# Performance work log

Hardware: AMD Instinct MI355X
Metric: run time of the kernel (lower is better)

The kernel has to match this reference:

```python
import jax, jax.numpy as jnp
import numpy as np

N = 50000       # nodes
E = 600000      # edges (before self-loops)
D_IN, D_H, D_OUT, D_E = 128, 128, 64, 8
NEG_SLOPE = 0.2


def _glorot(key, shape):
    fan = shape[0]
    return jax.random.normal(key, shape, dtype=jnp.float32) / jnp.sqrt(jnp.float32(fan))


def setup_inputs() -> dict:
    key = jax.random.key(0)
    ks = iter(jax.random.split(key, 32))
    inp = {
        "x": jax.random.normal(next(ks), (N, D_IN), dtype=jnp.float32),
        "edge_index": jax.random.randint(next(ks), (2, E), 0, N, dtype=jnp.int64),
        "edge_attr": jax.random.normal(next(ks), (E, D_E), dtype=jnp.float32),
    }
    dims = [(D_IN, D_H), (D_H, D_H), (D_H, D_OUT)]  # 3 GATConv layers, heads=1
    for i, (din, dout) in enumerate(dims):
        inp[f"W{i}"] = _glorot(next(ks), (din, dout))
        inp[f"as{i}"] = _glorot(next(ks), (dout,))
        inp[f"ad{i}"] = _glorot(next(ks), (dout,))
        inp[f"We{i}"] = _glorot(next(ks), (D_E, dout))
        inp[f"ae{i}"] = _glorot(next(ks), (dout,))
        inp[f"b{i}"] = jnp.zeros((dout,), dtype=jnp.float32)
    return inp


def _add_self_loops(src, dst, edge_attr, n):
    # PyG add_self_loops(fill_value='mean'): self-loop attr = mean of incoming edge attrs
    deg = jax.ops.segment_sum(jnp.ones_like(dst, dtype=edge_attr.dtype), dst, num_segments=n)
    mean_attr = jax.ops.segment_sum(edge_attr, dst, num_segments=n) / jnp.maximum(deg, 1.0)[:, None]
    loop = jnp.arange(n, dtype=src.dtype)
    return (jnp.concatenate([src, loop]),
            jnp.concatenate([dst, loop]),
            jnp.concatenate([edge_attr, mean_attr], axis=0))


def _gat_layer(x, src, dst, edge_attr, W, a_s, a_d, We, a_e, b, n):
    h = x @ W                                   # [N, C] linear projection
    alpha = (h @ a_s)[src] + (h @ a_d)[dst] + (edge_attr @ We) @ a_e   # [Etot]
    alpha = jax.nn.leaky_relu(alpha, NEG_SLOPE)
    m = jax.ops.segment_max(alpha, dst, num_segments=n)                # segment softmax over dst
    ex = jnp.exp(alpha - m[dst])
    denom = jax.ops.segment_sum(ex, dst, num_segments=n)
    w = ex / (denom[dst] + 1e-16)
    return jax.ops.segment_sum(h[src] * w[:, None], dst, num_segments=n) + b


def reference(x, edge_index, edge_attr,
              W0, as0, ad0, We0, ae0, b0,
              W1, as1, ad1, We1, ae1, b1,
              W2, as2, ad2, We2, ae2, b2):
    n = x.shape[0]
    src, dst, ea = _add_self_loops(edge_index[0], edge_index[1], edge_attr, n)
    h = jax.nn.relu(_gat_layer(x, src, dst, ea, W0, as0, ad0, We0, ae0, b0, n))
    h = jax.nn.relu(_gat_layer(h, src, dst, ea, W1, as1, ad1, We1, ae1, b1, n))
    return _gat_layer(h, src, dst, ea, W2, as2, ad2, We2, ae2, b2, n)
```

## Files before the change

kernel.cpp:

```cpp
#include <hip/hip_runtime.h>
#include <hip/hip_fp16.h>
#include <cstdint>

#define NEG_SLOPE 0.2f
#define LOG2E 1.4426950408889634f
#define MAXD 64


__global__ void k_zero(int* __restrict__ p, int n) {
    int i = blockIdx.x * blockDim.x + threadIdx.x;
    if (i < n) p[i] = 0;
}

__global__ void k_count_fill(const int* __restrict__ src, const int* __restrict__ dst,
                             const float* __restrict__ ea,
                             const float* __restrict__ We0, const float* __restrict__ ae0,
                             const float* __restrict__ We1, const float* __restrict__ ae1,
                             const float* __restrict__ We2, const float* __restrict__ ae2,
                             int* __restrict__ deg, ushort4* __restrict__ ed, int E) {
    __shared__ float swea[24];
    int tid = threadIdx.x;
    if (tid < 24) {
        int layer = tid >> 3, k = tid & 7;
        const float* We = layer == 0 ? We0 : (layer == 1 ? We1 : We2);
        const float* ae = layer == 0 ? ae0 : (layer == 1 ? ae1 : ae2);
        int D = layer == 2 ? 64 : 128;
        float s = 0.f;
        for (int t = 0; t < D; t++) s = fmaf(We[(size_t)k * D + t], ae[t], s);
        swea[tid] = s;
    }
    __syncthreads();
    int e = blockIdx.x * blockDim.x + tid;
    if (e >= E) return;
    int s = src[e];
    int d = dst[e];
    int r = atomicAdd(deg + d, 1);
    if (r > MAXD - 1) r = MAXD - 1;
    float4 a0 = *(const float4*)&ea[(size_t)e * 8];
    float4 a1 = *(const float4*)&ea[(size_t)e * 8 + 4];
    float4 w00 = *(const float4*)&swea[0],  w01 = *(const float4*)&swea[4];
    float4 w10 = *(const float4*)&swea[8],  w11 = *(const float4*)&swea[12];
    float4 w20 = *(const float4*)&swea[16], w21 = *(const float4*)&swea[20];
    float d0 = a0.x*w00.x + a0.y*w00.y + a0.z*w00.z + a0.w*w00.w
             + a1.x*w01.x + a1.y*w01.y + a1.z*w01.z + a1.w*w01.w;
    float d1 = a0.x*w10.x + a0.y*w10.y + a0.z*w10.z + a0.w*w10.w
             + a1.x*w11.x + a1.y*w11.y + a1.z*w11.z + a1.w*w11.w;
    float d2 = a0.x*w20.x + a0.y*w20.y + a0.z*w20.z + a0.w*w20.w
             + a1.x*w21.x + a1.y*w21.y + a1.z*w21.z + a1.w*w21.w;
    ushort4 rec;
    rec.x = (unsigned short)s;
    rec.y = __half_as_ushort(__float2half(d0));
    rec.z = __half_as_ushort(__float2half(d1));
    rec.w = __half_as_ushort(__float2half(d2));
    ed[(size_t)d * MAXD + r] = rec;
}


template<int DIN, int DOUT, bool XHALF>
__global__ __launch_bounds__(256) void k_gemm_dots(
    const void* __restrict__ Xv_, const float* __restrict__ W,
    const float* __restrict__ as_, const float* __restrict__ ad_,
    __half* __restrict__ H, float* __restrict__ hs, float* __restrict__ hd, int n)
{
    constexpr int GROUP = DOUT / 4;
    constexpr int BM = 4096 / DOUT;
    constexpr int KT = 32;
    __shared__ float sX[BM * KT];
    __shared__ float sW[KT * DOUT];

    int tid = threadIdx.x;
    int row_base = blockIdx.x * BM;
    int rows_avail = n - row_base; if (rows_avail > BM) rows_avail = BM;

    int r0 = (tid / GROUP) * 4;
    int c0 = (tid % GROUP) * 4;

    float acc[4][4] = {};

    for (int kt = 0; kt < DIN; kt += KT) {
        {
            constexpr int XV = BM * KT / 4;
            float4* sXv = (float4*)sX;
#pragma unroll
            for (int i = tid; i < XV; i += 256) {
                int row = i / (KT / 4), cc = i % (KT / 4);
                if (row < rows_avail) {
                    if constexpr (XHALF) {
                        const __half* Xh = (const __half*)Xv_;
                        uint2 raw = *(const uint2*)&Xh[(size_t)(row_base + row) * DIN + kt + cc * 4];
                        float2 f0 = __half22float2(*(__half2*)&raw.x);
                        float2 f1 = __half22float2(*(__half2*)&raw.y);
                        float4 v = { f0.x, f0.y, f1.x, f1.y };
                        sXv[i] = v;
                    } else {
                        const float* Xf = (const float*)Xv_;
                        sXv[i] = *(const float4*)&Xf[(size_t)(row_base + row) * DIN + kt + cc * 4];
                    }
                }
            }
        }
        {
            constexpr int WV = KT * DOUT / 4;
            float4* sWv = (float4*)sW;
            const float4* Wv = (const float4*)(W + (size_t)kt * DOUT);
#pragma unroll
            for (int i = tid; i < WV; i += 256) sWv[i] = Wv[i];
        }
        __syncthreads();

#pragma unroll 8
        for (int k = 0; k < KT; k++) {
            float4 w = *(const float4*)&sW[k * DOUT + c0];
            float xv[4];
#pragma unroll
            for (int i = 0; i < 4; i++) xv[i] = sX[(r0 + i) * KT + k];
#pragma unroll
            for (int i = 0; i < 4; i++) {
                acc[i][0] = fmaf(xv[i], w.x, acc[i][0]);
                acc[i][1] = fmaf(xv[i], w.y, acc[i][1]);
                acc[i][2] = fmaf(xv[i], w.z, acc[i][2]);
                acc[i][3] = fmaf(xv[i], w.w, acc[i][3]);
            }
        }
        __syncthreads();
    }

    float4 av = *(const float4*)&as_[c0];
    float4 dv = *(const float4*)&ad_[c0];

#pragma unroll
    for (int i = 0; i < 4; i++) {
        int row = row_base + r0 + i;
        bool ok = row < n;
        if (ok) {
            __half2 p0 = __floats2half2_rn(acc[i][0], acc[i][1]);
            __half2 p1 = __floats2half2_rn(acc[i][2], acc[i][3]);
            __half2* dst2 = (__half2*)&H[(size_t)row * DOUT + c0];
            dst2[0] = p0;
            dst2[1] = p1;
        }
        float ps = acc[i][0] * av.x + acc[i][1] * av.y + acc[i][2] * av.z + acc[i][3] * av.w;
        float pd = acc[i][0] * dv.x + acc[i][1] * dv.y + acc[i][2] * dv.z + acc[i][3] * dv.w;
#pragma unroll
        for (int off = GROUP / 2; off; off >>= 1) {
            ps += __shfl_xor(ps, off);
            pd += __shfl_xor(pd, off);
        }
        if (ok && (tid % GROUP) == 0) { hs[row] = ps; hd[row] = pd; }
    }
}


template<int CPL>
__device__ __forceinline__ void accum_row16(float* acc, const __half* __restrict__ hrow,
                                            int l, float w) {
    if constexpr (CPL == 8) {
        float4 raw = *(const float4*)(hrow + 8 * l);
        __half2* h = (__half2*)&raw;
#pragma unroll
        for (int i = 0; i < 4; i++) {
            float2 f = __half22float2(h[i]);
            acc[2 * i]     = fmaf(w, f.x, acc[2 * i]);
            acc[2 * i + 1] = fmaf(w, f.y, acc[2 * i + 1]);
        }
    } else {
        float2 raw = *(const float2*)(hrow + 4 * l);
        __half2* h = (__half2*)&raw;
#pragma unroll
        for (int i = 0; i < 2; i++) {
            float2 f = __half22float2(h[i]);
            acc[2 * i]     = fmaf(w, f.x, acc[2 * i]);
            acc[2 * i + 1] = fmaf(w, f.y, acc[2 * i + 1]);
        }
    }
}

__device__ __forceinline__ float unpack_w(unsigned int p) {
    return __half2float(__ushort_as_half((unsigned short)(p & 0xFFFFu)));
}

__device__ __forceinline__ float fexp(float x) {
    return exp2f(x * LOG2E);
}

template<int DOUT, bool RELU, int LCOMP, bool OUT_HALF>
__global__ void k_aggregate(const __half* __restrict__ H,
                            const int* __restrict__ deg, const ushort4* __restrict__ edata,
                            const float* __restrict__ hs, const float* __restrict__ hd,
                            const float* __restrict__ bias, void* __restrict__ out_, int n) {
    int t = blockIdx.x * blockDim.x + threadIdx.x;
    int wid = t >> 6, lane = t & 63;
    if (wid >= n) return;
    int d = deg[wid]; if (d > MAXD) d = MAXD;
    int start = wid << 6;
    int quarter = lane >> 4, l = lane & 15;
    float hdv = hd[wid];
    float hsw = hs[wid];

    constexpr int CPL = DOUT / 16;
    float acc[CPL] = {};

    float al = -3.0e38f; int s = 0; float eadv = 0.f;
    if (lane < d) {
        ushort4 pv = edata[start + lane];
        s = pv.x;
        unsigned short eu = (LCOMP == 1) ? pv.y : (LCOMP == 2) ? pv.z : pv.w;
        eadv = __half2float(__ushort_as_half(eu));
        float a = hs[s] + hdv + eadv;
        al = a > 0.f ? a : NEG_SLOPE * a;
    }
    float esum = (lane < d) ? eadv : 0.f;
    float m0 = al;
#pragma unroll
    for (int off = 32; off; off >>= 1) {
        esum += __shfl_xor(esum, off);
        m0 = fmaxf(m0, __shfl_xor(m0, off));
    }
    int dd = d < 1 ? 1 : d;
    float aself = hsw + hdv + esum / (float)dd;
    aself = aself > 0.f ? aself : NEG_SLOPE * aself;
    float m = fmaxf(m0, aself);

    float ex = (lane < d) ? fexp(al - m) : 0.f;
    float exsum = ex;
#pragma unroll
    for (int off = 32; off; off >>= 1) exsum += __shfl_xor(exsum, off);
    float exself = fexp(aself - m);
    float denom = exsum + exself;

    unsigned int pk = ((unsigned int)s << 16) |
                      (unsigned int)__half_as_ushort(__float2half(ex));

    if (quarter == 0) accum_row16<CPL>(acc, H + (size_t)wid * DOUT, l, exself);

    int quads = (d + 3) >> 2;
#pragma unroll 4
    for (int jj = 0; jj < quads; jj++) {
        int j = 4 * jj + quarter;
        unsigned int pj = (unsigned int)__shfl((int)pk, j);
        int sj = pj >> 16;
        float w = unpack_w(pj);
        if (j < d) accum_row16<CPL>(acc, H + ((size_t)sj << (CPL == 8 ? 7 : 6)), l, w);
    }

#pragma unroll
    for (int v = 0; v < CPL; v++) {
        acc[v] += __shfl_xor(acc[v], 16);
        acc[v] += __shfl_xor(acc[v], 32);
    }

    if (lane < 16) {
        float inv = 1.0f / (denom + 1e-16f);
        float o[CPL];
#pragma unroll
        for (int v = 0; v < CPL; v++) {
            o[v] = acc[v] * inv + bias[CPL * l + v];
            if (RELU) o[v] = fmaxf(o[v], 0.f);
        }
        if constexpr (OUT_HALF) {
            __half* outh = (__half*)out_;
            __half2 p[CPL / 2];
#pragma unroll
            for (int v = 0; v < CPL / 2; v++) p[v] = __floats2half2_rn(o[2 * v], o[2 * v + 1]);
            if constexpr (CPL == 8) {
                *(uint4*)&outh[(size_t)wid * DOUT + 8 * l] = *(uint4*)p;
            } else {
                *(uint2*)&outh[(size_t)wid * DOUT + 4 * l] = *(uint2*)p;
            }
        } else {
            float* outf = (float*)out_;
            if constexpr (CPL == 8) {
                float4 o0 = { o[0], o[1], o[2], o[3] };
                float4 o1 = { o[4], o[5], o[6], o[7] };
                *(float4*)&outf[(size_t)wid * DOUT + 8 * l] = o0;
                *(float4*)&outf[(size_t)wid * DOUT + 8 * l + 4] = o1;
            } else {
                float4 ov = { o[0], o[1], o[2], o[3] };
                *(float4*)&outf[(size_t)wid * DOUT + 4 * l] = ov;
            }
        }
    }
}


extern "C" void kernel_launch(void* const* d_in, const int* in_sizes, int n_in,
                              void* d_out, int out_size, void* d_ws, size_t ws_size,
                              hipStream_t stream) {
    const float* x     = (const float*)d_in[0];
    const int*   eidx  = (const int*)d_in[1];
    const float* eattr = (const float*)d_in[2];
    const int N = in_sizes[0] / 128;
    const int E = in_sizes[1] / 2;
    const int* src = eidx;
    const int* dst = eidx + E;

    char* ws = (char*)d_ws;
    size_t off = 0;
    auto alloc = [&](size_t bytes) -> void* {
        void* p = ws + off;
        off += (bytes + 255) & ~(size_t)255;
        return p;
    };
    __half*  bufA = (__half*)alloc((size_t)N * 128 * sizeof(__half));
    __half*  hbuf = (__half*)alloc((size_t)N * 128 * sizeof(__half));
    int*     deg  = (int*)alloc((size_t)N * sizeof(int));
    float*   hs   = (float*)alloc((size_t)N * sizeof(float));
    float*   hd   = (float*)alloc((size_t)N * sizeof(float));
    ushort4* ed   = (ushort4*)alloc((size_t)N * MAXD * sizeof(ushort4));

    const int tb = 256;

    k_zero<<<(N + tb - 1) / tb, tb, 0, stream>>>(deg, N);
    k_count_fill<<<(E + tb - 1) / tb, tb, 0, stream>>>(
        src, dst, eattr,
        (const float*)d_in[6], (const float*)d_in[7],
        (const float*)d_in[12], (const float*)d_in[13],
        (const float*)d_in[18], (const float*)d_in[19],
        deg, ed, E);

    int nwave_blocks = (N * 64 + tb - 1) / tb;

    {
        const float* W   = (const float*)d_in[3];
        const float* as_ = (const float*)d_in[4];
        const float* ad_ = (const float*)d_in[5];
        const float* b   = (const float*)d_in[8];
        k_gemm_dots<128, 128, false><<<(N + 31) / 32, 256, 0, stream>>>(x, W, as_, ad_, hbuf, hs, hd, N);
        k_aggregate<128, true, 1, true><<<nwave_blocks, tb, 0, stream>>>(hbuf, deg, ed, hs, hd, b, bufA, N);
    }
    {
        const float* W   = (const float*)d_in[9];
        const float* as_ = (const float*)d_in[10];
        const float* ad_ = (const float*)d_in[11];
        const float* b   = (const float*)d_in[14];
        k_gemm_dots<128, 128, true><<<(N + 31) / 32, 256, 0, stream>>>(bufA, W, as_, ad_, hbuf, hs, hd, N);
        k_aggregate<128, true, 2, true><<<nwave_blocks, tb, 0, stream>>>(hbuf, deg, ed, hs, hd, b, bufA, N);
    }
    {
        const float* W   = (const float*)d_in[15];
        const float* as_ = (const float*)d_in[16];
        const float* ad_ = (const float*)d_in[17];
        const float* b   = (const float*)d_in[20];
        k_gemm_dots<128, 64, true><<<(N + 63) / 64, 256, 0, stream>>>(bufA, W, as_, ad_, hbuf, hs, hd, N);
        k_aggregate<64, false, 3, false><<<nwave_blocks, tb, 0, stream>>>(hbuf, deg, ed, hs, hd, b, d_out, N);
    }
}
```

Baseline: 246.3 us.

## Split edge count/fill kernels and process eight neighbors per aggregation wave step

```diff
diff --git a/kernel.cpp b/kernel.cpp
--- a/kernel.cpp
+++ b/kernel.cpp
@@ -12,12 +12,22 @@
     if (i < n) p[i] = 0;
 }
 
-__global__ void k_count_fill(const int* __restrict__ src, const int* __restrict__ dst,
-                             const float* __restrict__ ea,
-                             const float* __restrict__ We0, const float* __restrict__ ae0,
-                             const float* __restrict__ We1, const float* __restrict__ ae1,
-                             const float* __restrict__ We2, const float* __restrict__ ae2,
-                             int* __restrict__ deg, ushort4* __restrict__ ed, int E) {
+__global__ void k_count(const int* __restrict__ dst, int* __restrict__ deg,
+                        unsigned short* __restrict__ rank, int E) {
+    int e = blockIdx.x * blockDim.x + threadIdx.x;
+    if (e < E) {
+        int r = atomicAdd(deg + dst[e], 1);
+        rank[e] = (unsigned short)(r > MAXD - 1 ? MAXD - 1 : r);
+    }
+}
+
+__global__ void k_fill(const int* __restrict__ src, const int* __restrict__ dst,
+                       const unsigned short* __restrict__ rank,
+                       const float* __restrict__ ea,
+                       const float* __restrict__ We0, const float* __restrict__ ae0,
+                       const float* __restrict__ We1, const float* __restrict__ ae1,
+                       const float* __restrict__ We2, const float* __restrict__ ae2,
+                       ushort4* __restrict__ ed, int E) {
     __shared__ float swea[24];
     int tid = threadIdx.x;
     if (tid < 24) {
@@ -33,9 +43,7 @@
     int e = blockIdx.x * blockDim.x + tid;
     if (e >= E) return;
     int s = src[e];
-    int d = dst[e];
-    int r = atomicAdd(deg + d, 1);
-    if (r > MAXD - 1) r = MAXD - 1;
+    int pos = dst[e] * MAXD + (int)rank[e];
     float4 a0 = *(const float4*)&ea[(size_t)e * 8];
     float4 a1 = *(const float4*)&ea[(size_t)e * 8 + 4];
     float4 w00 = *(const float4*)&swea[0],  w01 = *(const float4*)&swea[4];
@@ -52,7 +60,7 @@
     rec.y = __half_as_ushort(__float2half(d0));
     rec.z = __half_as_ushort(__float2half(d1));
     rec.w = __half_as_ushort(__float2half(d2));
-    ed[(size_t)d * MAXD + r] = rec;
+    ed[pos] = rec;
 }
 
 
@@ -152,23 +160,31 @@
 
 
 template<int CPL>
-__device__ __forceinline__ void accum_row16(float* acc, const __half* __restrict__ hrow,
-                                            int l, float w) {
-    if constexpr (CPL == 8) {
-        float4 raw = *(const float4*)(hrow + 8 * l);
-        __half2* h = (__half2*)&raw;
+__device__ __forceinline__ void accum_row8(float* acc, const __half* __restrict__ hrow,
+                                           int l, float w) {
+    if constexpr (CPL == 16) {
+        float4 r0 = *(const float4*)(hrow + 16 * l);
+        float4 r1 = *(const float4*)(hrow + 16 * l + 8);
+        __half2* h0 = (__half2*)&r0;
+        __half2* h1 = (__half2*)&r1;
 #pragma unroll
         for (int i = 0; i < 4; i++) {
-            float2 f = __half22float2(h[i]);
+            float2 f = __half22float2(h0[i]);
             acc[2 * i]     = fmaf(w, f.x, acc[2 * i]);
             acc[2 * i + 1] = fmaf(w, f.y, acc[2 * i + 1]);
         }
+#pragma unroll
+        for (int i = 0; i < 4; i++) {
+            float2 f = __half22float2(h1[i]);
+            acc[8 + 2 * i]     = fmaf(w, f.x, acc[8 + 2 * i]);
+            acc[8 + 2 * i + 1] = fmaf(w, f.y, acc[8 + 2 * i + 1]);
+        }
     } else {
-        float2 raw = *(const float2*)(hrow + 4 * l);
-        __half2* h = (__half2*)&raw;
-#pragma unroll
-        for (int i = 0; i < 2; i++) {
-            float2 f = __half22float2(h[i]);
+        float4 r0 = *(const float4*)(hrow + 8 * l);
+        __half2* h0 = (__half2*)&r0;
+#pragma unroll
+        for (int i = 0; i < 4; i++) {
+            float2 f = __half22float2(h0[i]);
             acc[2 * i]     = fmaf(w, f.x, acc[2 * i]);
             acc[2 * i + 1] = fmaf(w, f.y, acc[2 * i + 1]);
         }
@@ -193,11 +209,11 @@
     if (wid >= n) return;
     int d = deg[wid]; if (d > MAXD) d = MAXD;
     int start = wid << 6;
-    int quarter = lane >> 4, l = lane & 15;
+    int octet = lane >> 3, l = lane & 7;
     float hdv = hd[wid];
     float hsw = hs[wid];
 
-    constexpr int CPL = DOUT / 16;
+    constexpr int CPL = DOUT / 8;
     float acc[CPL] = {};
 
     float al = -3.0e38f; int s = 0; float eadv = 0.f;
@@ -231,25 +247,26 @@
     unsigned int pk = ((unsigned int)s << 16) |
                       (unsigned int)__half_as_ushort(__float2half(ex));
 
-    if (quarter == 0) accum_row16<CPL>(acc, H + (size_t)wid * DOUT, l, exself);
-
-    int quads = (d + 3) >> 2;
+    if (octet == 0) accum_row8<CPL>(acc, H + (size_t)wid * DOUT, l, exself);
+
+    int octs = (d + 7) >> 3;
 #pragma unroll 4
-    for (int jj = 0; jj < quads; jj++) {
-        int j = 4 * jj + quarter;
+    for (int jj = 0; jj < octs; jj++) {
+        int j = 8 * jj + octet;
         unsigned int pj = (unsigned int)__shfl((int)pk, j);
         int sj = pj >> 16;
         float w = unpack_w(pj);
-        if (j < d) accum_row16<CPL>(acc, H + ((size_t)sj << (CPL == 8 ? 7 : 6)), l, w);
+        if (j < d) accum_row8<CPL>(acc, H + ((size_t)sj << (CPL == 16 ? 7 : 6)), l, w);
     }
 
 #pragma unroll
     for (int v = 0; v < CPL; v++) {
+        acc[v] += __shfl_xor(acc[v], 8);
         acc[v] += __shfl_xor(acc[v], 16);
         acc[v] += __shfl_xor(acc[v], 32);
     }
 
-    if (lane < 16) {
+    if (lane < 8) {
         float inv = 1.0f / (denom + 1e-16f);
         float o[CPL];
 #pragma unroll
@@ -262,21 +279,18 @@
             __half2 p[CPL / 2];
 #pragma unroll
             for (int v = 0; v < CPL / 2; v++) p[v] = __floats2half2_rn(o[2 * v], o[2 * v + 1]);
-            if constexpr (CPL == 8) {
+            if constexpr (CPL == 16) {
+                *(uint4*)&outh[(size_t)wid * DOUT + 16 * l] = *(uint4*)p;
+                *(uint4*)&outh[(size_t)wid * DOUT + 16 * l + 8] = *(uint4*)(p + 4);
+            } else {
                 *(uint4*)&outh[(size_t)wid * DOUT + 8 * l] = *(uint4*)p;
-            } else {
-                *(uint2*)&outh[(size_t)wid * DOUT + 4 * l] = *(uint2*)p;
             }
         } else {
             float* outf = (float*)out_;
-            if constexpr (CPL == 8) {
-                float4 o0 = { o[0], o[1], o[2], o[3] };
-                float4 o1 = { o[4], o[5], o[6], o[7] };
-                *(float4*)&outf[(size_t)wid * DOUT + 8 * l] = o0;
-                *(float4*)&outf[(size_t)wid * DOUT + 8 * l + 4] = o1;
-            } else {
-                float4 ov = { o[0], o[1], o[2], o[3] };
-                *(float4*)&outf[(size_t)wid * DOUT + 4 * l] = ov;
+#pragma unroll
+            for (int v = 0; v < CPL / 4; v++) {
+                float4 ov = { o[4 * v], o[4 * v + 1], o[4 * v + 2], o[4 * v + 3] };
+                *(float4*)&outf[(size_t)wid * DOUT + CPL * l + 4 * v] = ov;
             }
         }
     }
@@ -301,22 +315,24 @@
         off += (bytes + 255) & ~(size_t)255;
         return p;
     };
-    __half*  bufA = (__half*)alloc((size_t)N * 128 * sizeof(__half));
-    __half*  hbuf = (__half*)alloc((size_t)N * 128 * sizeof(__half));
-    int*     deg  = (int*)alloc((size_t)N * sizeof(int));
-    float*   hs   = (float*)alloc((size_t)N * sizeof(float));
-    float*   hd   = (float*)alloc((size_t)N * sizeof(float));
-    ushort4* ed   = (ushort4*)alloc((size_t)N * MAXD * sizeof(ushort4));
+    __half*         bufA = (__half*)alloc((size_t)N * 128 * sizeof(__half));
+    __half*         hbuf = (__half*)alloc((size_t)N * 128 * sizeof(__half));
+    int*            deg  = (int*)alloc((size_t)N * sizeof(int));
+    float*          hs   = (float*)alloc((size_t)N * sizeof(float));
+    float*          hd   = (float*)alloc((size_t)N * sizeof(float));
+    ushort4*        ed   = (ushort4*)alloc((size_t)N * MAXD * sizeof(ushort4));
+    unsigned short* rank = (unsigned short*)alloc((size_t)E * sizeof(unsigned short));
 
     const int tb = 256;
 
     k_zero<<<(N + tb - 1) / tb, tb, 0, stream>>>(deg, N);
-    k_count_fill<<<(E + tb - 1) / tb, tb, 0, stream>>>(
-        src, dst, eattr,
+    k_count<<<(E + tb - 1) / tb, tb, 0, stream>>>(dst, deg, rank, E);
+    k_fill<<<(E + tb - 1) / tb, tb, 0, stream>>>(
+        src, dst, rank, eattr,
         (const float*)d_in[6], (const float*)d_in[7],
         (const float*)d_in[12], (const float*)d_in[13],
         (const float*)d_in[18], (const float*)d_in[19],
-        deg, ed, E);
+        ed, E);
 
     int nwave_blocks = (N * 64 + tb - 1) / tb;
 
```

Measured after the change: 264.6 us. 7.4% more time.

## Replace FP32 tiled GEMM with fp16 MFMA kernel using pre-transposed weights

Applied to the files above, without the earlier changes.

```diff
diff --git a/kernel.cpp b/kernel.cpp
--- a/kernel.cpp
+++ b/kernel.cpp
@@ -6,10 +6,30 @@
 #define LOG2E 1.4426950408889634f
 #define MAXD 64
 
+typedef _Float16 f16;
+typedef __attribute__((ext_vector_type(8))) _Float16 f16x8;
+typedef __attribute__((ext_vector_type(4))) float f32x4;
+
 
 __global__ void k_zero(int* __restrict__ p, int n) {
     int i = blockIdx.x * blockDim.x + threadIdx.x;
     if (i < n) p[i] = 0;
+}
+
+__global__ void k_wt(const float* __restrict__ W0, const float* __restrict__ W1,
+                     const float* __restrict__ W2, f16* __restrict__ Wt0,
+                     f16* __restrict__ Wt1, f16* __restrict__ Wt2) {
+    int i = blockIdx.x * 256 + threadIdx.x;
+    if (i < 16384) {
+        int k = i >> 7, c = i & 127;
+        Wt0[c * 128 + k] = (f16)W0[i];
+    } else if (i < 32768) {
+        int j = i - 16384; int k = j >> 7, c = j & 127;
+        Wt1[c * 128 + k] = (f16)W1[j];
+    } else if (i < 40960) {
+        int j = i - 32768; int k = j >> 6, c = j & 63;
+        Wt2[c * 128 + k] = (f16)W2[j];
+    }
 }
 
 __global__ void k_count_fill(const int* __restrict__ src, const int* __restrict__ dst,
@@ -56,97 +76,71 @@
 }
 
 
-template<int DIN, int DOUT, bool XHALF>
-__global__ __launch_bounds__(256) void k_gemm_dots(
-    const void* __restrict__ Xv_, const float* __restrict__ W,
+template<int DOUT, bool XHALF>
+__global__ __launch_bounds__(256) void k_gemm_mfma(
+    const void* __restrict__ X_, const f16* __restrict__ Wt,
     const float* __restrict__ as_, const float* __restrict__ ad_,
     __half* __restrict__ H, float* __restrict__ hs, float* __restrict__ hd, int n)
 {
-    constexpr int GROUP = DOUT / 4;
-    constexpr int BM = 4096 / DOUT;
-    constexpr int KT = 32;
-    __shared__ float sX[BM * KT];
-    __shared__ float sW[KT * DOUT];
-
-    int tid = threadIdx.x;
-    int row_base = blockIdx.x * BM;
-    int rows_avail = n - row_base; if (rows_avail > BM) rows_avail = BM;
-
-    int r0 = (tid / GROUP) * 4;
-    int c0 = (tid % GROUP) * 4;
-
-    float acc[4][4] = {};
-
-    for (int kt = 0; kt < DIN; kt += KT) {
-        {
-            constexpr int XV = BM * KT / 4;
-            float4* sXv = (float4*)sX;
-#pragma unroll
-            for (int i = tid; i < XV; i += 256) {
-                int row = i / (KT / 4), cc = i % (KT / 4);
-                if (row < rows_avail) {
-                    if constexpr (XHALF) {
-                        const __half* Xh = (const __half*)Xv_;
-                        uint2 raw = *(const uint2*)&Xh[(size_t)(row_base + row) * DIN + kt + cc * 4];
-                        float2 f0 = __half22float2(*(__half2*)&raw.x);
-                        float2 f1 = __half22float2(*(__half2*)&raw.y);
-                        float4 v = { f0.x, f0.y, f1.x, f1.y };
-                        sXv[i] = v;
-                    } else {
-                        const float* Xf = (const float*)Xv_;
-                        sXv[i] = *(const float4*)&Xf[(size_t)(row_base + row) * DIN + kt + cc * 4];
-                    }
-                }
+    constexpr int NT = DOUT / 16;
+    int lane = threadIdx.x & 63;
+    int wave = threadIdx.x >> 6;
+    int row0 = (blockIdx.x * 4 + wave) * 16;
+    if (row0 >= n) return;
+    int lrow = lane & 15;
+    int kgrp = lane >> 4;
+    int arow = row0 + lrow;
+    bool aok = arow < n;
+
+    f32x4 acc[NT] = {};
+
+#pragma unroll
+    for (int kt = 0; kt < 128; kt += 32) {
+        f16x8 a = {};
+        if (aok) {
+            if constexpr (XHALF) {
+                a = *(const f16x8*)((const f16*)X_ + (size_t)arow * 128 + kt + 8 * kgrp);
+            } else {
+                const float* xp = (const float*)X_ + (size_t)arow * 128 + kt + 8 * kgrp;
+                float4 x0 = *(const float4*)xp;
+                float4 x1 = *(const float4*)(xp + 4);
+                f16x8 t = { (f16)x0.x, (f16)x0.y, (f16)x0.z, (f16)x0.w,
+                            (f16)x1.x, (f16)x1.y, (f16)x1.z, (f16)x1.w };
+                a = t;
             }
         }
-        {
-            constexpr int WV = KT * DOUT / 4;
-            float4* sWv = (float4*)sW;
-            const float4* Wv = (const float4*)(W + (size_t)kt * DOUT);
-#pragma unroll
-            for (int i = tid; i < WV; i += 256) sWv[i] = Wv[i];
-        }
-        __syncthreads();
-
-#pragma unroll 8
-        for (int k = 0; k < KT; k++) {
-            float4 w = *(const float4*)&sW[k * DOUT + c0];
-            float xv[4];
-#pragma unroll
-            for (int i = 0; i < 4; i++) xv[i] = sX[(r0 + i) * KT + k];
-#pragma unroll
-            for (int i = 0; i < 4; i++) {
-                acc[i][0] = fmaf(xv[i], w.x, acc[i][0]);
-                acc[i][1] = fmaf(xv[i], w.y, acc[i][1]);
-                acc[i][2] = fmaf(xv[i], w.z, acc[i][2]);
-                acc[i][3] = fmaf(xv[i], w.w, acc[i][3]);
-            }
-        }
-        __syncthreads();
-    }
-
-    float4 av = *(const float4*)&as_[c0];
-    float4 dv = *(const float4*)&ad_[c0];
-
-#pragma unroll
-    for (int i = 0; i < 4; i++) {
-        int row = row_base + r0 + i;
-        bool ok = row < n;
-        if (ok) {
-            __half2 p0 = __floats2half2_rn(acc[i][0], acc[i][1]);
-            __half2 p1 = __floats2half2_rn(acc[i][2], acc[i][3]);
-            __half2* dst2 = (__half2*)&H[(size_t)row * DOUT + c0];
-            dst2[0] = p0;
-            dst2[1] = p1;
-        }
-        float ps = acc[i][0] * av.x + acc[i][1] * av.y + acc[i][2] * av.z + acc[i][3] * av.w;
-        float pd = acc[i][0] * dv.x + acc[i][1] * dv.y + acc[i][2] * dv.z + acc[i][3] * dv.w;
-#pragma unroll
-        for (int off = GROUP / 2; off; off >>= 1) {
+#pragma unroll
+        for (int nt = 0; nt < NT; nt++) {
+            f16x8 b = *(const f16x8*)(Wt + (size_t)(nt * 16 + lrow) * 128 + kt + 8 * kgrp);
+            acc[nt] = __builtin_amdgcn_mfma_f32_16x16x32_f16(a, b, acc[nt], 0, 0, 0);
+        }
+    }
+
+    float asv[NT], adv[NT];
+#pragma unroll
+    for (int nt = 0; nt < NT; nt++) {
+        asv[nt] = as_[nt * 16 + lrow];
+        adv[nt] = ad_[nt * 16 + lrow];
+    }
+
+#pragma unroll
+    for (int r = 0; r < 4; r++) {
+        int row = row0 + 4 * kgrp + r;
+        bool rok = row < n;
+        float ps = 0.f, pd = 0.f;
+#pragma unroll
+        for (int nt = 0; nt < NT; nt++) {
+            float v = acc[nt][r];
+            ps = fmaf(v, asv[nt], ps);
+            pd = fmaf(v, adv[nt], pd);
+            if (rok) H[(size_t)row * DOUT + nt * 16 + lrow] = __float2half(v);
+        }
+#pragma unroll
+        for (int off = 8; off; off >>= 1) {
             ps += __shfl_xor(ps, off);
             pd += __shfl_xor(pd, off);
         }
-        if (ok && (tid % GROUP) == 0) { hs[row] = ps; hd[row] = pd; }
+        if (rok && lrow == 0) { hs[row] = ps; hd[row] = pd; }
     }
 }
 
@@ -307,10 +301,15 @@
     float*   hs   = (float*)alloc((size_t)N * sizeof(float));
     float*   hd   = (float*)alloc((size_t)N * sizeof(float));
     ushort4* ed   = (ushort4*)alloc((size_t)N * MAXD * sizeof(ushort4));
+    f16*     Wt0  = (f16*)alloc(16384 * sizeof(f16));
+    f16*     Wt1  = (f16*)alloc(16384 * sizeof(f16));
+    f16*     Wt2  = (f16*)alloc(8192 * sizeof(f16));
 
     const int tb = 256;
 
     k_zero<<<(N + tb - 1) / tb, tb, 0, stream>>>(deg, N);
+    k_wt<<<160, 256, 0, stream>>>((const float*)d_in[3], (const float*)d_in[9],
+                                  (const float*)d_in[15], Wt0, Wt1, Wt2);
     k_count_fill<<<(E + tb - 1) / tb, tb, 0, stream>>>(
         src, dst, eattr,
         (const float*)d_in[6], (const float*)d_in[7],
@@ -319,29 +318,27 @@
         deg, ed, E);
 
     int nwave_blocks = (N * 64 + tb - 1) / tb;
+    int gemm_blocks = (N + 63) / 64;
 
     {
-        const float* W   = (const float*)d_in[3];
         const float* as_ = (const float*)d_in[4];
         const float* ad_ = (const float*)d_in[5];
         const float* b   = (const float*)d_in[8];
-        k_gemm_dots<128, 128, false><<<(N + 31) / 32, 256, 0, stream>>>(x, W, as_, ad_, hbuf, hs, hd, N);
+        k_gemm_mfma<128, false><<<gemm_blocks, 256, 0, stream>>>(x, Wt0, as_, ad_, hbuf, hs, hd, N);
         k_aggregate<128, true, 1, true><<<nwave_blocks, tb, 0, stream>>>(hbuf, deg, ed, hs, hd, b, bufA, N);
     }
     {
-        const float* W   = (const float*)d_in[9];
         const float* as_ = (const float*)d_in[10];
         const float* ad_ = (const float*)d_in[11];
         const float* b   = (const float*)d_in[14];
-        k_gemm_dots<128, 128, true><<<(N + 31) / 32, 256, 0, stream>>>(bufA, W, as_, ad_, hbuf, hs, hd, N);
+        k_gemm_mfma<128, true><<<gemm_blocks, 256, 0, stream>>>(bufA, Wt1, as_, ad_, hbuf, hs, hd, N);
         k_aggregate<128, true, 2, true><<<nwave_blocks, tb, 0, stream>>>(hbuf, deg, ed, hs, hd, b, bufA, N);
     }
     {
-        const float* W   = (const float*)d_in[15];
         const float* as_ = (const float*)d_in[16];
         const float* ad_ = (const float*)d_in[17];
         const float* b   = (const float*)d_in[20];
-        k_gemm_dots<128, 64, true><<<(N + 63) / 64, 256, 0, stream>>>(bufA, W, as_, ad_, hbuf, hs, hd, N);
+        k_gemm_mfma<64, true><<<gemm_blocks, 256, 0, stream>>>(bufA, Wt2, as_, ad_, hbuf, hs, hd, N);
         k_aggregate<64, false, 3, false><<<nwave_blocks, tb, 0, stream>>>(hbuf, deg, ed, hs, hd, b, d_out, N);
     }
 }
```

Result: faster. 226.8 us (-7.9%).
